# Kernel optimization log

Hardware: AMD Instinct MI355X
Metric: run time of the kernel (lower is better)

Reference implementation:

```python
import jax, jax.numpy as jnp
import numpy as np

N = 131072  # nodes processed in one frontier/level batch
H = 256     # h_size
X = 256     # x_size


def setup_inputs() -> dict:
    key = jax.random.key(0)
    ks = jax.random.split(key, 8)
    def w(k, shape, fan_in):
        return jax.random.normal(k, shape, jnp.float32) / np.float32(np.sqrt(fan_in))
    return {
        "x": jax.random.normal(ks[0], (N, X), jnp.float32),
        "child_h": jax.random.normal(ks[1], (N, H), jnp.float32),
        "child_c": jax.random.normal(ks[2], (N, H), jnp.float32),
        "child_idx": jax.random.randint(ks[3], (N,), 0, N, jnp.int32),
        "W_iou_w": w(ks[4], (3 * H, X), X),
        "U_iou_w": w(ks[5], (3 * H, H), H),
        "b_iou": jnp.zeros((1, 3 * H), jnp.float32),
        "W_f_w": w(ks[6], (H, X), X),
        "W_f_b": jnp.zeros((H,), jnp.float32),
        "U_f_w": w(ks[7], (H, H), H),
        "U_f_b": jnp.zeros((H,), jnp.float32),
        "b_f": jnp.zeros((1, H), jnp.float32),
    }


def reference(x, child_h, child_c, child_idx, W_iou_w, U_iou_w, b_iou,
              W_f_w, W_f_b, U_f_w, U_f_b, b_f):
    # Node-local projections (precomputed 'Wx' / 'Wfx' node data in the DGL module)
    Wx = x @ W_iou_w.T                      # [N, 3H]
    Wfx = x @ W_f_w.T + W_f_b               # [N, H] (nn.Linear bias included)
    # message_func + mailbox gather (one child per node; see shape analysis)
    hc = child_h[child_idx]                 # [N, H] irregular gather
    cc = child_c[child_idx]                 # [N, H]
    # reduce_func: forget gate + masked sum over children (K=1)
    f = jax.nn.sigmoid(Wfx + hc @ U_f_w.T + U_f_b + b_f)  # [N, H]
    c_red = f * cc                          # sum over 1 child
    iou = Wx + b_iou + hc @ U_iou_w.T       # [N, 3H]
    # apply_node_func: gated combine
    i, o, u = jnp.split(iou, 3, axis=1)
    c = jax.nn.sigmoid(i) * jnp.tanh(u) + c_red
    h = jax.nn.sigmoid(o) * jnp.tanh(c)
    return h, c
```

## Files before the change

kernel.cpp:

```cpp
#include <hip/hip_runtime.h>


typedef unsigned short u16;
typedef unsigned int u32;
typedef __bf16 bf16x8 __attribute__((ext_vector_type(8)));
typedef float f32x16 __attribute__((ext_vector_type(16)));
typedef u16 u16x4 __attribute__((ext_vector_type(4)));
typedef u16 u16x8 __attribute__((ext_vector_type(8)));

#define NTOT 131072
#define NHOFF (131072 * 256)

__device__ __forceinline__ u16 f2bf(float f) {
  u32 u = __float_as_uint(f);
  return (u16)((u + 0x7FFFu + ((u >> 16) & 1u)) >> 16);
}

__global__ void prep_w(const float* __restrict__ Wiou, const float* __restrict__ Uiou,
                       const float* __restrict__ Wf, const float* __restrict__ Uf,
                       u16* __restrict__ Bpack) {
  int cid = blockIdx.x * 256 + threadIdx.x;
  int j = cid >> 6;
  int kc = cid & 63;
  int k = kc * 8;
  int kt = kc >> 3, k8 = kc & 7;
  int s = j >> 8, g = (j >> 6) & 3, e = j & 63;
  int c = s * 64 + e;
  const float* src;
  if (j < 768) src = (k < 256) ? (Wiou + j * 256 + k) : (Uiou + j * 256 + (k - 256));
  else { int jj = j - 768; src = (k < 256) ? (Wf + jj * 256 + k) : (Uf + jj * 256 + (k - 256)); }
  float4 f0 = *(const float4*)(src);
  float4 f1 = *(const float4*)(src + 4);
  u16x8 v;
  v[0] = f2bf(f0.x); v[1] = f2bf(f0.y); v[2] = f2bf(f0.z); v[3] = f2bf(f0.w);
  v[4] = f2bf(f1.x); v[5] = f2bf(f1.y); v[6] = f2bf(f1.z); v[7] = f2bf(f1.w);
  int slot = (g * 8 + kt) * 2048 + ((c * 8 + k8) ^ (c & 7));
  *(u16x8*)(Bpack + slot * 8) = v;
}

__global__ void prep_bias(const float* __restrict__ biou, const float* __restrict__ wfb,
                          const float* __restrict__ ufb, const float* __restrict__ bfv,
                          float* __restrict__ Bias) {
  int j = blockIdx.x * 256 + threadIdx.x;
  Bias[j] = (j < 768) ? biou[j] : (wfb[j - 768] + ufb[j - 768] + bfv[j - 768]);
}

__global__ __launch_bounds__(256, 2)
void treelstm_main(const float* __restrict__ x, const float* __restrict__ child_h,
                   const float* __restrict__ child_c, const int* __restrict__ cidx,
                   const u16* __restrict__ Bpack, const float* __restrict__ Bias,
                   float* __restrict__ out) {
  __shared__ __align__(16) u16 ldsA[128 * 64];
  __shared__ __align__(16) u16 ldsB[256 * 64];
  __shared__ int lds_cidx[128];

  const int tid = threadIdx.x;
  const int n0 = blockIdx.x * 128;
  const int g = blockIdx.y;

  if (tid < 128) lds_cidx[tid] = cidx[n0 + tid];

  const int lane = tid & 63, w = tid >> 6;
  const int wm = w >> 1, wn = w & 1;
  const int lr = lane & 31, hi = lane >> 5;

  f32x16 acc[2][4] = {};

  const char* ldsAb = (const char*)ldsA;
  const char* ldsBb = (const char*)ldsB;
  int arow[2];
  #pragma unroll
  for (int mi = 0; mi < 2; mi++) arow[mi] = (wm * 64 + mi * 32 + lr) * 128;
  const int aswz = (lr & 7) << 4;
  int brow[4];
  #pragma unroll
  for (int s = 0; s < 4; s++) brow[s] = (s * 64 + wn * 32 + lr) * 128;
  const int bswz = (lr & 7) << 4;

  for (int kt = 0; kt < 8; ++kt) {
    #pragma unroll
    for (int q = 0; q < 8; ++q) {
      int v = q * 256 + tid;
      int r = v >> 4;
      int kq = (v & 15) * 4;
      const float* src = (kt < 4) ? (x + (n0 + r) * 256 + kt * 64 + kq)
                                  : (child_h + lds_cidx[r] * 256 + (kt - 4) * 64 + kq);
      float4 d = *(const float4*)src;
      u16x4 b;
      b[0] = f2bf(d.x); b[1] = f2bf(d.y); b[2] = f2bf(d.z); b[3] = f2bf(d.w);
      int addr = (r * 128 + kq * 2) ^ ((r & 7) << 4);
      *(u16x4*)((char*)ldsA + addr) = b;
    }
    const u16* bsrc = Bpack + (g * 8 + kt) * 16384;
    #pragma unroll
    for (int q = 0; q < 8; ++q) {
      int m = q * 256 + tid;
      *(u16x8*)((char*)ldsB + m * 16) = *(const u16x8*)(bsrc + m * 8);
    }
    __syncthreads();
    #pragma unroll
    for (int ks = 0; ks < 4; ++ks) {
      int kb = ks * 32 + hi * 16;
      bf16x8 af[2], bfr[4];
      #pragma unroll
      for (int mi = 0; mi < 2; mi++)
        af[mi] = *(const bf16x8*)(ldsAb + ((arow[mi] + kb) ^ aswz));
      #pragma unroll
      for (int s = 0; s < 4; s++)
        bfr[s] = *(const bf16x8*)(ldsBb + ((brow[s] + kb) ^ bswz));
      #pragma unroll
      for (int mi = 0; mi < 2; mi++)
        #pragma unroll
        for (int s = 0; s < 4; s++)
          acc[mi][s] = __builtin_amdgcn_mfma_f32_32x32x16_bf16(af[mi], bfr[s], acc[mi][s], 0, 0, 0);
    }
    __syncthreads();
  }

  const int tcol = g * 64 + wn * 32 + lr;
  const float bi = Bias[tcol], bo = Bias[256 + tcol], bu = Bias[512 + tcol], bfg = Bias[768 + tcol];
  #pragma unroll
  for (int mi = 0; mi < 2; mi++) {
    #pragma unroll
    for (int reg = 0; reg < 16; ++reg) {
      int row = wm * 64 + mi * 32 + (reg & 3) + 8 * (reg >> 2) + 4 * hi;
      int n = n0 + row;
      float i_ = acc[mi][0][reg] + bi;
      float o_ = acc[mi][1][reg] + bo;
      float u_ = acc[mi][2][reg] + bu;
      float fp = acc[mi][3][reg] + bfg;
      float ccv = child_c[lds_cidx[row] * 256 + tcol];
      float sigi = 1.f / (1.f + __expf(-i_));
      float sigo = 1.f / (1.f + __expf(-o_));
      float sigf = 1.f / (1.f + __expf(-fp));
      float tu = 2.f / (1.f + __expf(-2.f * u_)) - 1.f;
      float c = sigi * tu + sigf * ccv;
      float tc = 2.f / (1.f + __expf(-2.f * c)) - 1.f;
      out[n * 256 + tcol] = sigo * tc;
      out[NHOFF + n * 256 + tcol] = c;
    }
  }
}

extern "C" void kernel_launch(void* const* d_in, const int* in_sizes, int n_in,
                              void* d_out, int out_size, void* d_ws, size_t ws_size,
                              hipStream_t stream) {
  const float* x    = (const float*)d_in[0];
  const float* ch   = (const float*)d_in[1];
  const float* cc   = (const float*)d_in[2];
  const int*   ci   = (const int*)d_in[3];
  const float* Wiou = (const float*)d_in[4];
  const float* Uiou = (const float*)d_in[5];
  const float* biou = (const float*)d_in[6];
  const float* Wf   = (const float*)d_in[7];
  const float* Wfb  = (const float*)d_in[8];
  const float* Uf   = (const float*)d_in[9];
  const float* Ufb  = (const float*)d_in[10];
  const float* bfv  = (const float*)d_in[11];

  u16* Bpack = (u16*)d_ws;
  float* Bias = (float*)((char*)d_ws + (1 << 20));

  prep_w<<<256, 256, 0, stream>>>(Wiou, Uiou, Wf, Uf, Bpack);
  prep_bias<<<4, 256, 0, stream>>>(biou, Wfb, Ufb, bfv, Bias);
  dim3 grid(1024, 4);
  treelstm_main<<<grid, 256, 0, stream>>>(x, ch, cc, ci, Bpack, Bias, (float*)d_out);
}
```

Measured before the change: 397.2 us.

## Pre-pack gathered activations to bf16 and stream tiles via global_load_lds

```diff
diff --git a/kernel.cpp b/kernel.cpp
--- a/kernel.cpp
+++ b/kernel.cpp
@@ -45,11 +45,24 @@
   Bias[j] = (j < 768) ? biou[j] : (wfb[j - 768] + ufb[j - 768] + bfv[j - 768]);
 }
 
+__global__ void prep_apack(const float* __restrict__ x, const float* __restrict__ ch,
+                           const int* __restrict__ cidx, u16* __restrict__ Apack) {
+  int e = blockIdx.x * 256 + threadIdx.x;
+  int n = e >> 6, c = e & 63;
+  const float* src = (c < 32) ? (x + (size_t)n * 256 + c * 8)
+                              : (ch + (size_t)cidx[n] * 256 + (c - 32) * 8);
+  float4 f0 = *(const float4*)src;
+  float4 f1 = *(const float4*)(src + 4);
+  u16x8 v;
+  v[0] = f2bf(f0.x); v[1] = f2bf(f0.y); v[2] = f2bf(f0.z); v[3] = f2bf(f0.w);
+  v[4] = f2bf(f1.x); v[5] = f2bf(f1.y); v[6] = f2bf(f1.z); v[7] = f2bf(f1.w);
+  *(u16x8*)(Apack + (size_t)n * 512 + c * 8) = v;
+}
+
 __global__ __launch_bounds__(256, 2)
-void treelstm_main(const float* __restrict__ x, const float* __restrict__ child_h,
-                   const float* __restrict__ child_c, const int* __restrict__ cidx,
-                   const u16* __restrict__ Bpack, const float* __restrict__ Bias,
-                   float* __restrict__ out) {
+void treelstm_main_bf16(const u16* __restrict__ Apack, const u16* __restrict__ Bpack,
+                        const float* __restrict__ Bias, const float* __restrict__ child_c,
+                        const int* __restrict__ cidx, float* __restrict__ out) {
   __shared__ __align__(16) u16 ldsA[128 * 64];
   __shared__ __align__(16) u16 ldsB[256 * 64];
   __shared__ int lds_cidx[128];
@@ -66,6 +79,14 @@
 
   f32x16 acc[2][4] = {};
 
+  const char* aP = (const char*)Apack
+      + (size_t)(n0 + w * 32 + (lane >> 3)) * 1024
+      + (((lane & 7) ^ ((lane >> 3) & 7)) << 4);
+  const char* bP = (const char*)Bpack + (size_t)g * 262144 + ((w * 512 + lane) << 4);
+
+  char* ldsAw = (char*)ldsA + w * 4096;
+  char* ldsBw = (char*)ldsB + w * 8192;
+
   const char* ldsAb = (const char*)ldsA;
   const char* ldsBb = (const char*)ldsB;
   int arow[2];
@@ -77,26 +98,18 @@
   for (int s = 0; s < 4; s++) brow[s] = (s * 64 + wn * 32 + lr) * 128;
   const int bswz = (lr & 7) << 4;
 
+  #pragma unroll 1
   for (int kt = 0; kt < 8; ++kt) {
     #pragma unroll
-    for (int q = 0; q < 8; ++q) {
-      int v = q * 256 + tid;
-      int r = v >> 4;
-      int kq = (v & 15) * 4;
-      const float* src = (kt < 4) ? (x + (n0 + r) * 256 + kt * 64 + kq)
-                                  : (child_h + lds_cidx[r] * 256 + (kt - 4) * 64 + kq);
-      float4 d = *(const float4*)src;
-      u16x4 b;
-      b[0] = f2bf(d.x); b[1] = f2bf(d.y); b[2] = f2bf(d.z); b[3] = f2bf(d.w);
-      int addr = (r * 128 + kq * 2) ^ ((r & 7) << 4);
-      *(u16x4*)((char*)ldsA + addr) = b;
-    }
-    const u16* bsrc = Bpack + (g * 8 + kt) * 16384;
-    #pragma unroll
-    for (int q = 0; q < 8; ++q) {
-      int m = q * 256 + tid;
-      *(u16x8*)((char*)ldsB + m * 16) = *(const u16x8*)(bsrc + m * 8);
-    }
+    for (int q = 0; q < 4; ++q)
+      __builtin_amdgcn_global_load_lds(
+          (const __attribute__((address_space(1))) void*)(aP + q * 8192),
+          (__attribute__((address_space(3))) void*)(ldsAw + q * 1024), 16, 0, 0);
+    #pragma unroll
+    for (int q = 0; q < 8; ++q)
+      __builtin_amdgcn_global_load_lds(
+          (const __attribute__((address_space(1))) void*)(bP + q * 1024),
+          (__attribute__((address_space(3))) void*)(ldsBw + q * 1024), 16, 0, 0);
     __syncthreads();
     #pragma unroll
     for (int ks = 0; ks < 4; ++ks) {
@@ -115,6 +128,8 @@
           acc[mi][s] = __builtin_amdgcn_mfma_f32_32x32x16_bf16(af[mi], bfr[s], acc[mi][s], 0, 0, 0);
     }
     __syncthreads();
+    aP += 128;
+    bP += 32768;
   }
 
   const int tcol = g * 64 + wn * 32 + lr;
@@ -129,15 +144,112 @@
       float o_ = acc[mi][1][reg] + bo;
       float u_ = acc[mi][2][reg] + bu;
       float fp = acc[mi][3][reg] + bfg;
-      float ccv = child_c[lds_cidx[row] * 256 + tcol];
+      float ccv = child_c[(size_t)lds_cidx[row] * 256 + tcol];
       float sigi = 1.f / (1.f + __expf(-i_));
       float sigo = 1.f / (1.f + __expf(-o_));
       float sigf = 1.f / (1.f + __expf(-fp));
       float tu = 2.f / (1.f + __expf(-2.f * u_)) - 1.f;
       float c = sigi * tu + sigf * ccv;
       float tc = 2.f / (1.f + __expf(-2.f * c)) - 1.f;
-      out[n * 256 + tcol] = sigo * tc;
-      out[NHOFF + n * 256 + tcol] = c;
+      out[(size_t)n * 256 + tcol] = sigo * tc;
+      out[NHOFF + (size_t)n * 256 + tcol] = c;
+    }
+  }
+}
+
+__global__ __launch_bounds__(256, 2)
+void treelstm_main_f32(const float* __restrict__ x, const float* __restrict__ child_h,
+                       const float* __restrict__ child_c, const int* __restrict__ cidx,
+                       const u16* __restrict__ Bpack, const float* __restrict__ Bias,
+                       float* __restrict__ out) {
+  __shared__ __align__(16) u16 ldsA[128 * 64];
+  __shared__ __align__(16) u16 ldsB[256 * 64];
+  __shared__ int lds_cidx[128];
+
+  const int tid = threadIdx.x;
+  const int n0 = blockIdx.x * 128;
+  const int g = blockIdx.y;
+
+  if (tid < 128) lds_cidx[tid] = cidx[n0 + tid];
+
+  const int lane = tid & 63, w = tid >> 6;
+  const int wm = w >> 1, wn = w & 1;
+  const int lr = lane & 31, hi = lane >> 5;
+
+  f32x16 acc[2][4] = {};
+
+  const char* ldsAb = (const char*)ldsA;
+  const char* ldsBb = (const char*)ldsB;
+  int arow[2];
+  #pragma unroll
+  for (int mi = 0; mi < 2; mi++) arow[mi] = (wm * 64 + mi * 32 + lr) * 128;
+  const int aswz = (lr & 7) << 4;
+  int brow[4];
+  #pragma unroll
+  for (int s = 0; s < 4; s++) brow[s] = (s * 64 + wn * 32 + lr) * 128;
+  const int bswz = (lr & 7) << 4;
+
+  for (int kt = 0; kt < 8; ++kt) {
+    #pragma unroll
+    for (int q = 0; q < 8; ++q) {
+      int v = q * 256 + tid;
+      int r = v >> 4;
+      int kq = (v & 15) * 4;
+      const float* src = (kt < 4) ? (x + (size_t)(n0 + r) * 256 + kt * 64 + kq)
+                                  : (child_h + (size_t)lds_cidx[r] * 256 + (kt - 4) * 64 + kq);
+      float4 d = *(const float4*)src;
+      u16x4 b;
+      b[0] = f2bf(d.x); b[1] = f2bf(d.y); b[2] = f2bf(d.z); b[3] = f2bf(d.w);
+      int addr = (r * 128 + kq * 2) ^ ((r & 7) << 4);
+      *(u16x4*)((char*)ldsA + addr) = b;
+    }
+    const u16* bsrc = Bpack + (g * 8 + kt) * 16384;
+    #pragma unroll
+    for (int q = 0; q < 8; ++q) {
+      int m = q * 256 + tid;
+      *(u16x8*)((char*)ldsB + m * 16) = *(const u16x8*)(bsrc + m * 8);
+    }
+    __syncthreads();
+    #pragma unroll
+    for (int ks = 0; ks < 4; ++ks) {
+      int kb = ks * 32 + hi * 16;
+      bf16x8 af[2], bfr[4];
+      #pragma unroll
+      for (int mi = 0; mi < 2; mi++)
+        af[mi] = *(const bf16x8*)(ldsAb + ((arow[mi] + kb) ^ aswz));
+      #pragma unroll
+      for (int s = 0; s < 4; s++)
+        bfr[s] = *(const bf16x8*)(ldsBb + ((brow[s] + kb) ^ bswz));
+      #pragma unroll
+      for (int mi = 0; mi < 2; mi++)
+        #pragma unroll
+        for (int s = 0; s < 4; s++)
+          acc[mi][s] = __builtin_amdgcn_mfma_f32_32x32x16_bf16(af[mi], bfr[s], acc[mi][s], 0, 0, 0);
+    }
+    __syncthreads();
+  }
+
+  const int tcol = g * 64 + wn * 32 + lr;
+  const float bi = Bias[tcol], bo = Bias[256 + tcol], bu = Bias[512 + tcol], bfg = Bias[768 + tcol];
+  #pragma unroll
+  for (int mi = 0; mi < 2; mi++) {
+    #pragma unroll
+    for (int reg = 0; reg < 16; ++reg) {
+      int row = wm * 64 + mi * 32 + (reg & 3) + 8 * (reg >> 2) + 4 * hi;
+      int n = n0 + row;
+      float i_ = acc[mi][0][reg] + bi;
+      float o_ = acc[mi][1][reg] + bo;
+      float u_ = acc[mi][2][reg] + bu;
+      float fp = acc[mi][3][reg] + bfg;
+      float ccv = child_c[(size_t)lds_cidx[row] * 256 + tcol];
+      float sigi = 1.f / (1.f + __expf(-i_));
+      float sigo = 1.f / (1.f + __expf(-o_));
+      float sigf = 1.f / (1.f + __expf(-fp));
+      float tu = 2.f / (1.f + __expf(-2.f * u_)) - 1.f;
+      float c = sigi * tu + sigf * ccv;
+      float tc = 2.f / (1.f + __expf(-2.f * c)) - 1.f;
+      out[(size_t)n * 256 + tcol] = sigo * tc;
+      out[NHOFF + (size_t)n * 256 + tcol] = c;
     }
   }
 }
@@ -160,9 +272,18 @@
 
   u16* Bpack = (u16*)d_ws;
   float* Bias = (float*)((char*)d_ws + (1 << 20));
+  u16* Apack = (u16*)((char*)d_ws + (2 << 20));
+
+  const size_t need = (size_t)(2 << 20) + (size_t)NTOT * 512 * sizeof(u16);
 
   prep_w<<<256, 256, 0, stream>>>(Wiou, Uiou, Wf, Uf, Bpack);
   prep_bias<<<4, 256, 0, stream>>>(biou, Wfb, Ufb, bfv, Bias);
+
   dim3 grid(1024, 4);
-  treelstm_main<<<grid, 256, 0, stream>>>(x, ch, cc, ci, Bpack, Bias, (float*)d_out);
-}
+  if (ws_size >= need) {
+    prep_apack<<<32768, 256, 0, stream>>>(x, ch, ci, Apack);
+    treelstm_main_bf16<<<grid, 256, 0, stream>>>(Apack, Bpack, Bias, cc, ci, (float*)d_out);
+  } else {
+    treelstm_main_f32<<<grid, 256, 0, stream>>>(x, ch, cc, ci, Bpack, Bias, (float*)d_out);
+  }
+}
```

New measurement: 318.6 us. 1.25x faster.

## Pre-pack bf16 activations and use pipelined global_load_lds GEMM kernel

Applied to the files above, without the earlier changes.

```diff
diff --git a/kernel.cpp b/kernel.cpp
--- a/kernel.cpp
+++ b/kernel.cpp
@@ -4,21 +4,46 @@
 typedef unsigned short u16;
 typedef unsigned int u32;
 typedef __bf16 bf16x8 __attribute__((ext_vector_type(8)));
+typedef float f32x4 __attribute__((ext_vector_type(4)));
 typedef float f32x16 __attribute__((ext_vector_type(16)));
 typedef u16 u16x4 __attribute__((ext_vector_type(4)));
 typedef u16 u16x8 __attribute__((ext_vector_type(8)));
 
 #define NTOT 131072
-#define NHOFF (131072 * 256)
+#define NHOFF ((size_t)131072 * 256)
+#define AS1 __attribute__((address_space(1)))
+#define AS3 __attribute__((address_space(3)))
 
 __device__ __forceinline__ u16 f2bf(float f) {
   u32 u = __float_as_uint(f);
   return (u16)((u + 0x7FFFu + ((u >> 16) & 1u)) >> 16);
 }
 
-__global__ void prep_w(const float* __restrict__ Wiou, const float* __restrict__ Uiou,
-                       const float* __restrict__ Wf, const float* __restrict__ Uf,
-                       u16* __restrict__ Bpack) {
+__global__ void prep_w_v9(const float* __restrict__ Wiou, const float* __restrict__ Uiou,
+                          const float* __restrict__ Wf, const float* __restrict__ Uf,
+                          u16* __restrict__ Bpack) {
+  int cid = blockIdx.x * 256 + threadIdx.x;
+  int slot = cid & 2047;
+  int kt = (cid >> 11) & 7;
+  int g = cid >> 14;
+  int pcol = slot >> 3, c16 = slot & 7;
+  int wn = pcol >> 6, fc = (pcol >> 4) & 3, e16 = pcol & 15;
+  int j = fc * 256 + g * 64 + wn * 16 + e16;
+  int k0 = kt * 64 + (c16 ^ (pcol & 7)) * 8;
+  const float* src;
+  if (j < 768) src = (k0 < 256) ? (Wiou + (size_t)j * 256 + k0) : (Uiou + (size_t)j * 256 + (k0 - 256));
+  else { int jj = j - 768; src = (k0 < 256) ? (Wf + (size_t)jj * 256 + k0) : (Uf + (size_t)jj * 256 + (k0 - 256)); }
+  float4 f0 = *(const float4*)(src);
+  float4 f1 = *(const float4*)(src + 4);
+  u16x8 v;
+  v[0] = f2bf(f0.x); v[1] = f2bf(f0.y); v[2] = f2bf(f0.z); v[3] = f2bf(f0.w);
+  v[4] = f2bf(f1.x); v[5] = f2bf(f1.y); v[6] = f2bf(f1.z); v[7] = f2bf(f1.w);
+  *(u16x8*)(Bpack + (size_t)cid * 8) = v;
+}
+
+__global__ void prep_w_legacy(const float* __restrict__ Wiou, const float* __restrict__ Uiou,
+                              const float* __restrict__ Wf, const float* __restrict__ Uf,
+                              u16* __restrict__ Bpack) {
   int cid = blockIdx.x * 256 + threadIdx.x;
   int j = cid >> 6;
   int kc = cid & 63;
@@ -45,11 +70,161 @@
   Bias[j] = (j < 768) ? biou[j] : (wfb[j - 768] + ufb[j - 768] + bfv[j - 768]);
 }
 
+__global__ void prep_apack(const float* __restrict__ x, const float* __restrict__ ch,
+                           const int* __restrict__ cidx, u16* __restrict__ Apack) {
+  int e = blockIdx.x * 256 + threadIdx.x;
+  int n = e >> 6, c = e & 63;
+  const float* src = (c < 32) ? (x + (size_t)n * 256 + c * 8)
+                              : (ch + (size_t)cidx[n] * 256 + (c - 32) * 8);
+  float4 f0 = *(const float4*)src;
+  float4 f1 = *(const float4*)(src + 4);
+  u16x8 v;
+  v[0] = f2bf(f0.x); v[1] = f2bf(f0.y); v[2] = f2bf(f0.z); v[3] = f2bf(f0.w);
+  v[4] = f2bf(f1.x); v[5] = f2bf(f1.y); v[6] = f2bf(f1.z); v[7] = f2bf(f1.w);
+  *(u16x8*)(Apack + (size_t)n * 512 + c * 8) = v;
+}
+
+__global__ __launch_bounds__(512, 2)
+void treelstm_v10(const u16* __restrict__ Apack, const u16* __restrict__ Bpack,
+                  const float* __restrict__ Bias, const float* __restrict__ child_c,
+                  const int* __restrict__ cidx, float* __restrict__ out) {
+  __shared__ __align__(16) char lds[131072];
+  __shared__ int lds_cidx[256];
+
+  const int tid = threadIdx.x;
+  const int orig = blockIdx.x;
+  const int bid = (orig & 7) * 256 + (orig >> 3);
+  const int g = bid & 3;
+  const int n0 = (bid >> 2) * 256;
+  if (tid < 256) lds_cidx[tid] = cidx[n0 + tid];
+
+  const int l = tid & 63, w = tid >> 6;
+  const int wm = w >> 2, wn = w & 3;
+  const int l15 = l & 15, lhi = l >> 4;
+
+  const char* aSrc = (const char*)Apack + (size_t)(n0 + (tid >> 3)) * 1024
+                     + (((tid & 7) ^ ((tid >> 3) & 7)) << 4);
+  const char* bSrc = (const char*)Bpack + (size_t)g * 262144 + (size_t)tid * 16;
+
+  const int aBase = wm * 16384 + l15 * 128;
+  const int bBase = 65536 + wn * 8192 + l15 * 128;
+  int koff[2];
+  koff[0] = (lhi * 16) ^ ((l & 7) << 4);
+  koff[1] = (64 + lhi * 16) ^ ((l & 7) << 4);
+
+  f32x4 acc[8][4] = {};
+  bf16x8 a[4][2], b0[2][2], b1[2][2];
+
+  #define ST_A(KT, H)                                                              \
+    { __builtin_amdgcn_global_load_lds(                                            \
+          (const AS1 void*)(aSrc + (KT) * 128 + ((H) * 128 + 0) * 1024),           \
+          (AS3 void*)(lds + ((KT) & 1) * 32768 + (H) * 16384 + tid * 16), 16, 0, 0); \
+      __builtin_amdgcn_global_load_lds(                                            \
+          (const AS1 void*)(aSrc + (KT) * 128 + ((H) * 128 + 64) * 1024),          \
+          (AS3 void*)(lds + ((KT) & 1) * 32768 + (H) * 16384 + 8192 + tid * 16), 16, 0, 0); }
+  #define ST_B(KT, H)                                                              \
+    { __builtin_amdgcn_global_load_lds(                                            \
+          (const AS1 void*)(bSrc + (KT) * 32768 + (H) * 16384),                    \
+          (AS3 void*)(lds + 65536 + ((KT) & 1) * 32768 + (H) * 16384 + tid * 16), 16, 0, 0); \
+      __builtin_amdgcn_global_load_lds(                                            \
+          (const AS1 void*)(bSrc + (KT) * 32768 + (H) * 16384 + 8192),             \
+          (AS3 void*)(lds + 65536 + ((KT) & 1) * 32768 + (H) * 16384 + 8192 + tid * 16), 16, 0, 0); }
+
+  #define RD_A(PAR, FMB)                                                           \
+    { _Pragma("unroll") for (int i = 0; i < 4; ++i)                                \
+      _Pragma("unroll") for (int kh = 0; kh < 2; ++kh)                             \
+        a[i][kh] = *(const bf16x8*)(lds + (PAR) * 32768 + aBase + ((FMB) + i) * 2048 + koff[kh]); }
+  #define RD_B(D, PAR, FCB)                                                        \
+    { _Pragma("unroll") for (int i = 0; i < 2; ++i)                                \
+      _Pragma("unroll") for (int kh = 0; kh < 2; ++kh)                             \
+        D[i][kh] = *(const bf16x8*)(lds + (PAR) * 32768 + bBase + ((FCB) + i) * 2048 + koff[kh]); }
+
+  #define MM(B2, FMB, FCB)                                                         \
+    { __builtin_amdgcn_s_setprio(1);                                               \
+      _Pragma("unroll") for (int kh = 0; kh < 2; ++kh)                             \
+      _Pragma("unroll") for (int i = 0; i < 4; ++i)                                \
+      _Pragma("unroll") for (int j2 = 0; j2 < 2; ++j2)                             \
+        acc[(FMB) + i][(FCB) + j2] = __builtin_amdgcn_mfma_f32_16x16x32_bf16(      \
+            a[i][kh], B2[j2][kh], acc[(FMB) + i][(FCB) + j2], 0, 0, 0);            \
+      __builtin_amdgcn_s_setprio(0); }
+
+  #define BAR { __builtin_amdgcn_s_barrier(); __builtin_amdgcn_sched_barrier(0); }
+  #define LGKM0 { asm volatile("s_waitcnt lgkmcnt(0)" ::: "memory"); __builtin_amdgcn_sched_barrier(0); }
+  #define VM(N) { asm volatile("s_waitcnt vmcnt(" #N ")" ::: "memory"); __builtin_amdgcn_sched_barrier(0); }
+
+  ST_B(0, 0); ST_B(0, 1); ST_A(0, 0); ST_A(0, 1);
+  ST_B(1, 0); ST_B(1, 1); ST_A(1, 0);
+  VM(6); BAR;
+
+  #pragma unroll
+  for (int t = 0; t < 4; ++t) {
+    const int k1 = 2 * t + 1, k2 = 2 * t + 2, k3 = 2 * t + 3;
+    RD_A(0, 0); RD_B(b0, 0, 0);
+    ST_A(k1, 1);
+    BAR; LGKM0; MM(b0, 0, 0); BAR;
+    RD_B(b1, 0, 2);
+    BAR; LGKM0; MM(b1, 0, 2); BAR;
+    RD_A(0, 4);
+    if (t < 3) ST_B(k2, 0);
+    BAR; LGKM0; MM(b1, 4, 2); BAR;
+    if (t < 3) { ST_B(k2, 1); ST_A(k2, 0); }
+    BAR; MM(b0, 4, 0);
+    if (t < 3) { VM(6); } else { VM(0); }
+    BAR;
+    RD_A(1, 0); RD_B(b0, 1, 0);
+    if (t < 3) ST_A(k2, 1);
+    BAR; LGKM0; MM(b0, 0, 0); BAR;
+    RD_B(b1, 1, 2);
+    BAR; LGKM0; MM(b1, 0, 2); BAR;
+    RD_A(1, 4);
+    if (t < 3) { ST_B(k3, 0); ST_B(k3, 1); }
+    BAR; LGKM0; MM(b1, 4, 2); BAR;
+    if (t < 3) ST_A(k3, 0);
+    BAR; MM(b0, 4, 0);
+    if (t < 3) { VM(6); }
+    BAR;
+  }
+  #undef ST_A
+  #undef ST_B
+  #undef RD_A
+  #undef RD_B
+  #undef MM
+  #undef VM
+  #undef LGKM0
+  #undef BAR
+
+  const int hcol = g * 64 + wn * 16 + l15;
+  float b4[4];
+  #pragma unroll
+  for (int fc = 0; fc < 4; ++fc) b4[fc] = Bias[fc * 256 + hcol];
+  #pragma unroll
+  for (int fm = 0; fm < 8; ++fm) {
+    #pragma unroll
+    for (int reg = 0; reg < 4; ++reg) {
+      int rowl = wm * 128 + fm * 16 + lhi * 4 + reg;
+      size_t n = (size_t)(n0 + rowl);
+      float i_ = acc[fm][0][reg] + b4[0];
+      float o_ = acc[fm][1][reg] + b4[1];
+      float u_ = acc[fm][2][reg] + b4[2];
+      float fp = acc[fm][3][reg] + b4[3];
+      float ccv = child_c[(size_t)lds_cidx[rowl] * 256 + hcol];
+      float sigi = 1.f / (1.f + __expf(-i_));
+      float sigo = 1.f / (1.f + __expf(-o_));
+      float sigf = 1.f / (1.f + __expf(-fp));
+      float tu = 2.f / (1.f + __expf(-2.f * u_)) - 1.f;
+      float c = sigi * tu + sigf * ccv;
+      float tc = 2.f / (1.f + __expf(-2.f * c)) - 1.f;
+      out[n * 256 + hcol] = sigo * tc;
+      out[NHOFF + n * 256 + hcol] = c;
+    }
+  }
+}
+
 __global__ __launch_bounds__(256, 2)
-void treelstm_main(const float* __restrict__ x, const float* __restrict__ child_h,
-                   const float* __restrict__ child_c, const int* __restrict__ cidx,
-                   const u16* __restrict__ Bpack, const float* __restrict__ Bias,
-                   float* __restrict__ out) {
+void treelstm_main_f32(const float* __restrict__ x, const float* __restrict__ child_h,
+                       const float* __restrict__ child_c, const int* __restrict__ cidx,
+                       const u16* __restrict__ Bpack, const float* __restrict__ Bias,
+                       float* __restrict__ out) {
   __shared__ __align__(16) u16 ldsA[128 * 64];
   __shared__ __align__(16) u16 ldsB[256 * 64];
   __shared__ int lds_cidx[128];
@@ -83,8 +258,8 @@
       int v = q * 256 + tid;
       int r = v >> 4;
       int kq = (v & 15) * 4;
-      const float* src = (kt < 4) ? (x + (n0 + r) * 256 + kt * 64 + kq)
-                                  : (child_h + lds_cidx[r] * 256 + (kt - 4) * 64 + kq);
+      const float* src = (kt < 4) ? (x + (size_t)(n0 + r) * 256 + kt * 64 + kq)
+                                  : (child_h + (size_t)lds_cidx[r] * 256 + (kt - 4) * 64 + kq);
       float4 d = *(const float4*)src;
       u16x4 b;
       b[0] = f2bf(d.x); b[1] = f2bf(d.y); b[2] = f2bf(d.z); b[3] = f2bf(d.w);
@@ -129,15 +304,15 @@
       float o_ = acc[mi][1][reg] + bo;
       float u_ = acc[mi][2][reg] + bu;
       float fp = acc[mi][3][reg] + bfg;
-      float ccv = child_c[lds_cidx[row] * 256 + tcol];
+      float ccv = child_c[(size_t)lds_cidx[row] * 256 + tcol];
       float sigi = 1.f / (1.f + __expf(-i_));
       float sigo = 1.f / (1.f + __expf(-o_));
       float sigf = 1.f / (1.f + __expf(-fp));
       float tu = 2.f / (1.f + __expf(-2.f * u_)) - 1.f;
       float c = sigi * tu + sigf * ccv;
       float tc = 2.f / (1.f + __expf(-2.f * c)) - 1.f;
-      out[n * 256 + tcol] = sigo * tc;
-      out[NHOFF + n * 256 + tcol] = c;
+      out[(size_t)n * 256 + tcol] = sigo * tc;
+      out[NHOFF + (size_t)n * 256 + tcol] = c;
     }
   }
 }
@@ -160,9 +335,19 @@
 
   u16* Bpack = (u16*)d_ws;
   float* Bias = (float*)((char*)d_ws + (1 << 20));
-
-  prep_w<<<256, 256, 0, stream>>>(Wiou, Uiou, Wf, Uf, Bpack);
+  u16* Apack = (u16*)((char*)d_ws + (2 << 20));
+
+  const size_t need = (size_t)(2 << 20) + (size_t)NTOT * 512 * sizeof(u16);
+
   prep_bias<<<4, 256, 0, stream>>>(biou, Wfb, Ufb, bfv, Bias);
-  dim3 grid(1024, 4);
-  treelstm_main<<<grid, 256, 0, stream>>>(x, ch, cc, ci, Bpack, Bias, (float*)d_out);
-}
+
+  if (ws_size >= need) {
+    prep_w_v9<<<256, 256, 0, stream>>>(Wiou, Uiou, Wf, Uf, Bpack);
+    prep_apack<<<32768, 256, 0, stream>>>(x, ch, ci, Apack);
+    treelstm_v10<<<2048, 512, 0, stream>>>(Apack, Bpack, Bias, cc, ci, (float*)d_out);
+  } else {
+    prep_w_legacy<<<256, 256, 0, stream>>>(Wiou, Uiou, Wf, Uf, Bpack);
+    dim3 grid(1024, 4);
+    treelstm_main_f32<<<grid, 256, 0, stream>>>(x, ch, cc, ci, Bpack, Bias, (float*)d_out);
+  }
+}
```

New measurement: 334.4 us. 1.19x faster.
